# Performance work log

Hardware: AMD Instinct MI355X
Metric: run time of the kernel (lower is better)

Reference implementation:

```python
import jax, jax.numpy as jnp
import numpy as np

N_NODES = 40000
N_EDGES = 480000
MULT = 64
NUM_SPECIES = 5
N_BASIS = 8
MLP_HIDDEN = 64
AVG_NEIGH = 12.0

INV8 = float(1.0 / np.sqrt(8.0))
INV64 = float(1.0 / np.sqrt(64.0))
INV128 = float(1.0 / np.sqrt(128.0))


def _poly_envelope(x):
    # e3nn.poly_envelope(5, 2) == DimeNet-style cutoff with p=6:
    # f(0)=1, first 5 derivatives zero at 0, f and 2 derivatives zero at 1.
    u = 1.0 - 28.0 * x**6 + 48.0 * x**7 - 21.0 * x**8
    return jnp.where(x < 1.0, u, 0.0)


def setup_inputs() -> dict:
    key = jax.random.key(0)
    ks = jax.random.split(key, 15)
    vectors = jax.random.uniform(ks[0], (N_EDGES, 3), jnp.float32, -0.5, 0.5)
    node_scalars = jax.random.normal(ks[1], (N_NODES, MULT), jnp.float32)
    node_vectors = jax.random.normal(ks[2], (N_NODES, MULT, 3), jnp.float32)
    node_specie = jax.random.randint(ks[3], (N_NODES,), 0, NUM_SPECIES)
    senders = jax.random.randint(ks[4], (N_EDGES,), 0, N_NODES)
    receivers = jax.random.randint(ks[5], (N_EDGES,), 0, N_NODES)
    # learned params (e3nn Linear weights ~ N(0,1), fwd divides by sqrt(fan_in))
    W_up_s = jax.random.normal(ks[6], (MULT, MULT), jnp.float32)
    W_up_v = jax.random.normal(ks[7], (MULT, MULT), jnp.float32)
    W_skip_s = jax.random.normal(ks[8], (NUM_SPECIES, MULT, 2 * MULT), jnp.float32)
    W_skip_v = jax.random.normal(ks[9], (NUM_SPECIES, MULT, MULT), jnp.float32)
    W_mlp1 = jax.random.normal(ks[10], (N_BASIS, MLP_HIDDEN), jnp.float32)
    W_mlp2 = jax.random.normal(ks[11], (MLP_HIDDEN, MLP_HIDDEN), jnp.float32)
    W_mlp3 = jax.random.normal(ks[12], (MLP_HIDDEN, 4 * MULT), jnp.float32)
    W_down_s = jax.random.normal(ks[13], (2 * MULT, 2 * MULT), jnp.float32)
    W_down_v = jax.random.normal(ks[14], (2 * MULT, MULT), jnp.float32)
    return dict(vectors=vectors, node_scalars=node_scalars, node_vectors=node_vectors,
                node_specie=node_specie, senders=senders, receivers=receivers,
                W_up_s=W_up_s, W_up_v=W_up_v, W_skip_s=W_skip_s, W_skip_v=W_skip_v,
                W_mlp1=W_mlp1, W_mlp2=W_mlp2, W_mlp3=W_mlp3,
                W_down_s=W_down_s, W_down_v=W_down_v)


def reference(vectors, node_scalars, node_vectors, node_specie, senders, receivers,
              W_up_s, W_up_v, W_skip_s, W_skip_v, W_mlp1, W_mlp2, W_mlp3,
              W_down_s, W_down_v):
    N = node_scalars.shape[0]
    # self-connection: species-indexed linear ('skip_tp'), output 128x0e + 64x1o
    sc_s = jnp.einsum('ni,nio->no', node_scalars, W_skip_s[node_specie]) * INV64
    sc_v = jnp.einsum('nic,nio->noc', node_vectors, W_skip_v[node_specie]) * INV64
    # linear_up (irreps-wise linear, 64x0e+64x1o -> same)
    h_s = (node_scalars @ W_up_s) * INV64
    h_v = jnp.einsum('nic,io->noc', node_vectors, W_up_v) * INV64
    # gather by sender
    m_s = h_s[senders]                       # [E,64]
    m_v = h_v[senders]                       # [E,64,3]
    # spherical harmonics l=1, normalize=True, component norm: sqrt(3)*r_hat
    lengths = jnp.linalg.norm(vectors, axis=1, keepdims=True)   # [E,1]
    safe_len = jnp.where(lengths == 0.0, 1.0, lengths)
    Y = jnp.sqrt(3.0) * vectors / safe_len                      # [E,3]
    # sparse CG tensor product (component norm): 0e x 1o -> 1o, 1o x 1o -> 0e
    tp_1o = m_s[:, :, None] * Y[:, None, :]                     # [E,64,3]
    tp_0e = jnp.einsum('eic,ec->ei', m_v, Y) / jnp.sqrt(3.0)    # [E,64]
    # concatenate + regroup -> 128x0e + 128x1o
    msg_s = jnp.concatenate([m_s, tp_0e], axis=1)               # [E,128]
    msg_v = jnp.concatenate([m_v, tp_1o], axis=1)               # [E,128,3]
    # radial basis (bessel, x_max=1) * smooth envelope
    k = jnp.arange(1, N_BASIS + 1, dtype=jnp.float32)
    bes = jnp.sqrt(2.0) * jnp.sin(k * jnp.pi * safe_len) / safe_len  # [E,8]
    rb = jnp.where(lengths == 0.0, 0.0, bes * _poly_envelope(lengths))
    h = jax.nn.swish((rb @ W_mlp1) * INV8)
    h = jax.nn.swish((h @ W_mlp2) * INV64)
    mix = (h @ W_mlp3) * INV64                                  # [E,256]
    msg_s = msg_s * mix[:, :128]
    msg_v = msg_v * mix[:, 128:, None]
    # scatter-add to receivers, normalize by sqrt(avg_num_neighbors)
    inv_sqrt_nn = 1.0 / np.sqrt(AVG_NEIGH)
    agg_s = jax.ops.segment_sum(msg_s, receivers, num_segments=N) * inv_sqrt_nn
    agg_v = jax.ops.segment_sum(msg_v, receivers, num_segments=N) * inv_sqrt_nn
    # linear_down to 128x0e + 64x1o, plus self-connection
    d_s = (agg_s @ W_down_s) * INV128 + sc_s                    # [N,128]
    d_v = jnp.einsum('nic,io->noc', agg_v, W_down_v) * INV128 + sc_v  # [N,64,3]
    # gate: first 64 scalars kept (swish), last 64 gate the vectors (swish)
    out_s = jax.nn.swish(d_s[:, :MULT])
    gates = jax.nn.swish(d_s[:, MULT:])
    out_v = d_v * gates[:, :, None]
    return jnp.concatenate([out_s, out_v.reshape(N, MULT * 3)], axis=1)  # [N,256]
```

## Files before the change

### kernel.cpp

```cpp
#include <hip/hip_runtime.h>
#include <hip/hip_bf16.h>

#define N_NODES 40000
#define N_EDGES 480000
#define SEG 4
#define SEG_E (N_EDGES / SEG)
#define SEG_TILES (SEG_E / 16)
#define SCAN_BLOCKS 157

typedef short bf16x8 __attribute__((ext_vector_type(8)));
typedef float f32x4 __attribute__((ext_vector_type(4)));

__device__ __forceinline__ float bf2f(__hip_bfloat16 x) { return __bfloat162float(x); }

__device__ __forceinline__ float swishf(float x) { return x / (1.0f + __expf(-x)); }

__device__ __forceinline__ float bflo(unsigned u) { union { unsigned u; float f; } w; w.u = u << 16; return w.f; }
__device__ __forceinline__ float bfhi(unsigned u) { union { unsigned u; float f; } w; w.u = u & 0xffff0000u; return w.f; }
__device__ __forceinline__ float bfu(unsigned short u) { union { unsigned u; float f; } w; w.u = ((unsigned)u) << 16; return w.f; }

__device__ __forceinline__ unsigned short f2bf_bits(float x) {
    union { __hip_bfloat16 h; unsigned short u; } c; c.h = __float2bfloat16(x); return c.u;
}

__constant__ const float INV8 = 0.35355339059327373f;
__constant__ const float INV64 = 0.125f;
__constant__ const float INV128 = 0.08838834764831845f;
__constant__ const float INV_NN = 0.2886751345948129f;
__constant__ const float SQRT2 = 1.4142135623730951f;
__constant__ const float SQRT3 = 1.7320508075688772f;
__constant__ const float INV_SQRT3 = 0.5773502691896258f;
__constant__ const float PI_F = 3.14159265358979323846f;

template<bool F32>
__device__ __forceinline__ float LD(const void* p, int i) {
    if constexpr (F32) return ((const float*)p)[i];
    else return bf2f(((const __hip_bfloat16*)p)[i]);
}
template<bool F32>
__device__ __forceinline__ void ST(void* p, size_t i, float v) {
    if constexpr (F32) ((float*)p)[i] = v;
    else ((__hip_bfloat16*)p)[i] = __float2bfloat16(v);
}

template<bool F32>
__device__ __forceinline__ void load_f8(const void* p, size_t i, float* out) {
    if constexpr (F32) {
        const float4* q4 = (const float4*)((const float*)p + i);
        float4 a = q4[0], b = q4[1];
        out[0] = a.x; out[1] = a.y; out[2] = a.z; out[3] = a.w;
        out[4] = b.x; out[5] = b.y; out[6] = b.z; out[7] = b.w;
    } else {
        bf16x8 v = *(const bf16x8*)((const unsigned short*)p + i);
        #pragma unroll
        for (int j = 0; j < 8; j++) out[j] = bfu((unsigned short)v[j]);
    }
}

__global__ void detect_kernel(const unsigned short* __restrict__ w, int* __restrict__ flag) {
    int lane = threadIdx.x;
    int cnt = 0;
    for (int i = lane; i < 2048; i += 64) {
        unsigned e = (w[2 * i] >> 7) & 0xFF;
        if (e >= 110 && e <= 133) cnt++;
    }
    #pragma unroll
    for (int off = 32; off > 0; off >>= 1) cnt += __shfl_down(cnt, off, 64);
    if (lane == 0) *flag = (cnt > 1024) ? 1 : 0;
}

template<bool F32>
__global__ __launch_bounds__(256) void wprep_kernel(
    const void* __restrict__ W_up_s, const void* __restrict__ W_up_v,
    const void* __restrict__ W_skip_s, const void* __restrict__ W_skip_v,
    const void* __restrict__ W_down_s, const void* __restrict__ W_down_v,
    const void* __restrict__ W_mlp2, const void* __restrict__ W_mlp3,
    unsigned short* __restrict__ Wup_sq, unsigned short* __restrict__ Wup_vq,
    unsigned short* __restrict__ Wq_s, unsigned short* __restrict__ Wq_v,
    unsigned short* __restrict__ W2q, unsigned short* __restrict__ W3q,
    const int* __restrict__ flag)
{
    if ((*flag != 0) == F32) return;
    const float SC = INV128 * INV_NN;
    int gid = blockIdx.x * 256 + threadIdx.x;
    int gs = gridDim.x * 256;
    for (int i = gid; i < 4096; i += gs) {
        int o = i & 63, k = i >> 6;
        Wup_sq[o * 72 + k] = f2bf_bits(LD<F32>(W_up_s, k * 64 + o) * INV64);
        Wup_vq[o * 72 + k] = f2bf_bits(LD<F32>(W_up_v, k * 64 + o) * INV64);
    }
    for (int i = gid; i < 5 * 128 * 192; i += gs) {
        int sp = i / 24576, r = i - sp * 24576;
        int o = r / 192, k = r - o * 192;
        float w = (k < 128) ? LD<F32>(W_down_s, k * 128 + o) * SC
                            : LD<F32>(W_skip_s, sp * 8192 + (k - 128) * 128 + o) * INV64;
        Wq_s[sp * 25600 + o * 200 + k] = f2bf_bits(w);
    }
    for (int i = gid; i < 5 * 64 * 192; i += gs) {
        int sp = i / 12288, r = i - sp * 12288;
        int o = r / 192, k = r - o * 192;
        float w = (k < 128) ? LD<F32>(W_down_v, k * 64 + o) * SC
                            : LD<F32>(W_skip_v, sp * 4096 + (k - 128) * 64 + o) * INV64;
        Wq_v[sp * 12800 + o * 200 + k] = f2bf_bits(w);
    }
    for (int i = gid; i < 16384; i += gs) {
        int o = i & 255, k = i >> 8;
        W3q[o * 72 + k] = f2bf_bits(LD<F32>(W_mlp3, k * 256 + o));
    }
    for (int i = gid; i < 4096; i += gs) {
        int o = i & 63, k = i >> 6;
        W2q[o * 72 + k] = f2bf_bits(LD<F32>(W_mlp2, k * 64 + o));
    }
}

__global__ __launch_bounds__(256) void hist_kernel(const int* __restrict__ receivers,
                                                   int* __restrict__ cnt) {
    int e = blockIdx.x * 256 + threadIdx.x;
    if (e < N_EDGES) atomicAdd(&cnt[receivers[e]], 1);
}

__global__ __launch_bounds__(256) void partial_kernel(const int* __restrict__ cnt,
                                                      int* __restrict__ partials) {
    __shared__ int red[4];
    int idx = blockIdx.x * 256 + threadIdx.x;
    int v = (idx < N_NODES) ? cnt[idx] : 0;
    #pragma unroll
    for (int off = 32; off > 0; off >>= 1) v += __shfl_down(v, off, 64);
    int wave = threadIdx.x >> 6, lane = threadIdx.x & 63;
    if (lane == 0) red[wave] = v;
    __syncthreads();
    if (threadIdx.x == 0) partials[blockIdx.x] = red[0] + red[1] + red[2] + red[3];
}

__global__ __launch_bounds__(256) void scanp_kernel(const int* __restrict__ partials,
                                                    int* __restrict__ pscan) {
    __shared__ int buf[256];
    int t = threadIdx.x;
    int v = (t < SCAN_BLOCKS) ? partials[t] : 0;
    buf[t] = v;
    __syncthreads();
    for (int off = 1; off < 256; off <<= 1) {
        int tmp = (t >= off) ? buf[t - off] : 0;
        __syncthreads();
        buf[t] += tmp;
        __syncthreads();
    }
    if (t < SCAN_BLOCKS) pscan[t] = buf[t] - v;
}

__global__ __launch_bounds__(256) void offs_kernel(const int* __restrict__ cnt,
                                                   const int* __restrict__ pscan,
                                                   int* __restrict__ offs,
                                                   int* __restrict__ cursor) {
    __shared__ int buf[256];
    int b = blockIdx.x, t = threadIdx.x;
    int idx = b * 256 + t;
    int v = (idx < N_NODES) ? cnt[idx] : 0;
    buf[t] = v;
    __syncthreads();
    for (int off = 1; off < 256; off <<= 1) {
        int tmp = (t >= off) ? buf[t - off] : 0;
        __syncthreads();
        buf[t] += tmp;
        __syncthreads();
    }
    int exc = buf[t] - v + pscan[b];
    if (idx < N_NODES) { offs[idx] = exc; cursor[idx] = exc; }
    if (idx == N_NODES - 1) offs[N_NODES] = exc + v;
}

__global__ __launch_bounds__(256) void scatter_kernel(const int* __restrict__ receivers,
                                                      const int* __restrict__ senders,
                                                      int* __restrict__ cursor,
                                                      int* __restrict__ sorted_eid,
                                                      int* __restrict__ sorted_snd) {
    int e = blockIdx.x * 256 + threadIdx.x;
    if (e < N_EDGES) {
        int p = atomicAdd(&cursor[receivers[e]], 1);
        sorted_eid[p] = e;
        sorted_snd[p] = senders[e];
    }
}

__global__ __launch_bounds__(256) void hist5_kernel(const int* __restrict__ specie,
                                                    int* __restrict__ cnt5) {
    int n = blockIdx.x * 256 + threadIdx.x;
    int lane = threadIdx.x & 63;
    int sp = (n < N_NODES) ? specie[n] : -1;
    #pragma unroll
    for (int s = 0; s < 5; s++) {
        unsigned long long mask = __ballot(sp == s);
        if (mask != 0ull) {
            int leader = __builtin_ctzll(mask);
            if (lane == leader) atomicAdd(&cnt5[s], __popcll(mask));
        }
    }
}

__global__ void scan5_kernel(const int* __restrict__ cnt5, int* __restrict__ sp_offs,
                             int* __restrict__ cursor5, int* __restrict__ tile_info) {
    if (threadIdx.x != 0 || blockIdx.x != 0) return;
    int run = 0, tb = 0;
    for (int s = 0; s < 5; s++) {
        sp_offs[s] = run; cursor5[s] = run;
        tile_info[s] = tb;
        int c = cnt5[s];
        int T = (c + 15) >> 4;
        tile_info[8 + s] = T;
        tb += (T + 3) >> 2;
        run += c;
    }
    sp_offs[5] = run;
    tile_info[5] = tb;
}

__global__ __launch_bounds__(256) void scatter5_kernel(const int* __restrict__ specie,
                                                       int* __restrict__ cursor5,
                                                       int* __restrict__ sorted_node) {
    int n = blockIdx.x * 256 + threadIdx.x;
    int lane = threadIdx.x & 63;
    int sp = (n < N_NODES) ? specie[n] : -1;
    #pragma unroll
    for (int s = 0; s < 5; s++) {
        unsigned long long mask = __ballot(sp == s);
        if (mask != 0ull) {
            int leader = __builtin_ctzll(mask);
            int base = 0;
            if (lane == leader) base = atomicAdd(&cursor5[s], __popcll(mask));
            base = __shfl(base, leader);
            if (sp == s) {
                int prefix = __popcll(mask & ((1ull << lane) - 1ull));
                sorted_node[base + prefix] = n;
            }
        }
    }
}

template<bool F32>
__global__ __launch_bounds__(256) void node_up_kernel(
    const void* __restrict__ node_scalars,
    const void* __restrict__ node_vectors,
    const unsigned short* __restrict__ Wup_sq,
    const unsigned short* __restrict__ Wup_vq,
    unsigned short* __restrict__ hbuf,
    unsigned short* __restrict__ ns_b,
    unsigned short* __restrict__ nv_t,
    const int* __restrict__ flag)
{
    if ((*flag != 0) == F32) return;
    __shared__ __align__(16) unsigned short WsT[64 * 72];
    __shared__ __align__(16) unsigned short WvT[64 * 72];
    int tid = threadIdx.x;
    for (int i = tid; i < 576; i += 256) {
        ((uint4*)WsT)[i] = ((const uint4*)Wup_sq)[i];
        ((uint4*)WvT)[i] = ((const uint4*)Wup_vq)[i];
    }
    __syncthreads();
    int wave = tid >> 6, lane = tid & 63;
    int m = lane & 15, q = lane >> 4;
    int base = (blockIdx.x * 4 + wave) * 16;

    f32x4 accS[4];
    f32x4 accV[3][4];
    #pragma unroll
    for (int t = 0; t < 4; t++) {
        accS[t] = f32x4{0.f, 0.f, 0.f, 0.f};
        #pragma unroll
        for (int c = 0; c < 3; c++) accV[c][t] = f32x4{0.f, 0.f, 0.f, 0.f};
    }

    #pragma unroll
    for (int kk = 0; kk < 2; kk++) {
        int i0 = kk * 32 + 8 * q;
        float fs[8];
        load_f8<F32>(node_scalars, (size_t)(base + m) * 64 + i0, fs);
        bf16x8 aS;
        #pragma unroll
        for (int j = 0; j < 8; j++) aS[j] = (short)f2bf_bits(fs[j]);
        *(bf16x8*)(ns_b + (size_t)(base + m) * 64 + i0) = aS;
        float fv[24];
        size_t vbase = (size_t)(base + m) * 192 + (size_t)i0 * 3;
        load_f8<F32>(node_vectors, vbase,      fv);
        load_f8<F32>(node_vectors, vbase + 8,  fv + 8);
        load_f8<F32>(node_vectors, vbase + 16, fv + 16);
        bf16x8 aV[3];
        #pragma unroll
        for (int c = 0; c < 3; c++) {
            #pragma unroll
            for (int j = 0; j < 8; j++) aV[c][j] = (short)f2bf_bits(fv[3 * j + c]);
            *(bf16x8*)(nv_t + (size_t)c * N_NODES * 64 + (size_t)(base + m) * 64 + i0) = aV[c];
        }
        #pragma unroll
        for (int t = 0; t < 4; t++) {
            bf16x8 bS = *(const bf16x8*)(WsT + (16 * t + m) * 72 + kk * 32 + 8 * q);
            bf16x8 bV = *(const bf16x8*)(WvT + (16 * t + m) * 72 + kk * 32 + 8 * q);
            accS[t]    = __builtin_amdgcn_mfma_f32_16x16x32_bf16(aS,    bS, accS[t],    0, 0, 0);
            accV[0][t] = __builtin_amdgcn_mfma_f32_16x16x32_bf16(aV[0], bV, accV[0][t], 0, 0, 0);
            accV[1][t] = __builtin_amdgcn_mfma_f32_16x16x32_bf16(aV[1], bV, accV[1][t], 0, 0, 0);
            accV[2][t] = __builtin_amdgcn_mfma_f32_16x16x32_bf16(aV[2], bV, accV[2][t], 0, 0, 0);
        }
    }
    #pragma unroll
    for (int t = 0; t < 4; t++) {
        #pragma unroll
        for (int r = 0; r < 4; r++) {
            uint2 pk;
            pk.x = (unsigned)f2bf_bits(accS[t][r])    | ((unsigned)f2bf_bits(accV[0][t][r]) << 16);
            pk.y = (unsigned)f2bf_bits(accV[1][t][r]) | ((unsigned)f2bf_bits(accV[2][t][r]) << 16);
            *(uint2*)(hbuf + (size_t)(base + 4 * q + r) * 256 + (16 * t + m) * 4) = pk;
        }
    }
}

template<bool F32>
__global__ __launch_bounds__(512) void mlp_kernel(
    const void* __restrict__ vectors,
    const int* __restrict__ sorted_eid,
    const void* __restrict__ W1,
    const unsigned short* __restrict__ W2q,
    const unsigned short* __restrict__ W3q,
    unsigned short* __restrict__ mixseg,
    unsigned short* __restrict__ yq,
    int p_lo,
    const int* __restrict__ flag)
{
    if ((*flag != 0) == F32) return;
    __shared__ __align__(16) unsigned short W3T[256 * 72];
    __shared__ __align__(16) unsigned short W2T[64 * 72];
    __shared__ unsigned short hbl[8 * 64 * 17];
    int tid = threadIdx.x;
    for (int i = tid; i < 2304; i += 512) ((uint4*)W3T)[i] = ((const uint4*)W3q)[i];
    for (int i = tid; i < 576; i += 512)  ((uint4*)W2T)[i] = ((const uint4*)W2q)[i];
    __syncthreads();
    int wave = tid >> 6, lane = tid & 63;
    int m = lane & 15, q = lane >> 4;
    int tile = blockIdx.x * 8 + wave;
    if (tile >= SEG_TILES) return;
    int p = p_lo + tile * 16 + m;

    int e = sorted_eid[p];
    float vx = LD<F32>(vectors, e * 3 + 0);
    float vy = LD<F32>(vectors, e * 3 + 1);
    float vz = LD<F32>(vectors, e * 3 + 2);
    float len2 = vx * vx + vy * vy + vz * vz;
    float len = sqrtf(len2);
    float Yx = 0.f, Yy = 0.f, Yz = 0.f;
    float rb[8];
    if (len > 0.f) {
        float inv = 1.f / len;
        Yx = SQRT3 * vx * inv; Yy = SQRT3 * vy * inv; Yz = SQRT3 * vz * inv;
        float x6 = len2 * len2 * len2;
        float env = (len < 1.f) ? fmaf(x6, fmaf(len, fmaf(len, -21.f, 48.f), -28.f), 1.f) : 0.f;
        float c = SQRT2 * inv * env;
        #pragma unroll
        for (int k = 0; k < 8; k++) rb[k] = c * __sinf((float)(k + 1) * PI_F * len);
    } else {
        #pragma unroll
        for (int k = 0; k < 8; k++) rb[k] = 0.f;
    }
    if (q == 0) {
        uint2 yw;
        yw.x = f2bf_bits(Yx) | ((unsigned)f2bf_bits(Yy) << 16);
        yw.y = f2bf_bits(Yz);
        *(uint2*)(yq + (size_t)p * 4) = yw;
    }

    f32x4 zero4 = {0.f, 0.f, 0.f, 0.f};
    unsigned short* hb = hbl + wave * (64 * 17);

    bf16x8 b_rb;
    #pragma unroll
    for (int j = 0; j < 8; j++) b_rb[j] = (q == 0) ? (short)f2bf_bits(rb[j]) : (short)0;
    #pragma unroll
    for (int t = 0; t < 4; t++) {
        bf16x8 a;
        #pragma unroll
        for (int j = 0; j < 8; j++) a[j] = 0;
        if (q == 0) {
            #pragma unroll
            for (int j = 0; j < 8; j++)
                a[j] = (short)f2bf_bits(LD<F32>(W1, j * 64 + 16 * t + m));
        }
        f32x4 c = __builtin_amdgcn_mfma_f32_16x16x32_bf16(a, b_rb, zero4, 0, 0, 0);
        #pragma unroll
        for (int r = 0; r < 4; r++)
            hb[(16 * t + 4 * q + r) * 17 + m] = f2bf_bits(swishf(c[r] * INV8));
    }
    bf16x8 b2[2];
    #pragma unroll
    for (int h = 0; h < 2; h++)
        #pragma unroll
        for (int j = 0; j < 8; j++)
            b2[h][j] = (short)hb[(32 * h + 8 * q + j) * 17 + m];
    #pragma unroll
    for (int t = 0; t < 4; t++) {
        bf16x8 a0 = *(const bf16x8*)(W2T + (16 * t + m) * 72 + 8 * q);
        bf16x8 a1 = *(const bf16x8*)(W2T + (16 * t + m) * 72 + 32 + 8 * q);
        f32x4 c = __builtin_amdgcn_mfma_f32_16x16x32_bf16(a0, b2[0], zero4, 0, 0, 0);
        c = __builtin_amdgcn_mfma_f32_16x16x32_bf16(a1, b2[1], c, 0, 0, 0);
        #pragma unroll
        for (int r = 0; r < 4; r++)
            hb[(16 * t + 4 * q + r) * 17 + m] = f2bf_bits(swishf(c[r] * INV64));
    }
    bf16x8 b3[2];
    #pragma unroll
    for (int h = 0; h < 2; h++)
        #pragma unroll
        for (int j = 0; j < 8; j++)
            b3[h][j] = (short)hb[(32 * h + 8 * q + j) * 17 + m];
    size_t rowbase = ((size_t)(tile * 16 + m)) * 256;
    #pragma unroll
    for (int t3 = 0; t3 < 16; t3++) {
        bf16x8 a0 = *(const bf16x8*)(W3T + (16 * t3 + m) * 72 + 8 * q);
        bf16x8 a1 = *(const bf16x8*)(W3T + (16 * t3 + m) * 72 + 32 + 8 * q);
        f32x4 c = __builtin_amdgcn_mfma_f32_16x16x32_bf16(a0, b3[0], zero4, 0, 0, 0);
        c = __builtin_amdgcn_mfma_f32_16x16x32_bf16(a1, b3[1], c, 0, 0, 0);
        uint2 v;
        v.x = f2bf_bits(c[0] * INV64) | ((unsigned)f2bf_bits(c[1] * INV64) << 16);
        v.y = f2bf_bits(c[2] * INV64) | ((unsigned)f2bf_bits(c[3] * INV64) << 16);
        *(uint2*)(mixseg + rowbase + 16 * t3 + 4 * q) = v;
    }
}

__global__ __launch_bounds__(256) void agg_kernel(
    const unsigned short* __restrict__ hbuf,
    const int* __restrict__ sorted_snd,
    const unsigned short* __restrict__ mixseg,
    const unsigned short* __restrict__ yq,
    const int* __restrict__ offs,
    unsigned short* __restrict__ agg_s_b,
    unsigned short* __restrict__ agg_v_b,
    int slo, int shi)
{
    int tid = threadIdx.x, wave = tid >> 6, lane = tid & 63;
    int n = blockIdx.x * 4 + wave;
    if (n >= N_NODES) return;
    int beg = __builtin_amdgcn_readfirstlane(offs[n]);
    int end = __builtin_amdgcn_readfirstlane(offs[n + 1]);
    int lo = beg > slo ? beg : slo;
    int hi = end < shi ? end : shi;
    bool owner = (beg >= slo && beg < shi) || (beg >= shi && shi == N_EDGES);
    if (!owner && hi <= lo) return;
    unsigned short* aS = agg_s_b + (size_t)n * 128;
    unsigned short* aV = agg_v_b + (size_t)n * 384;
    float s0, s1, v0, v1, v2, v3, v4, v5;
    if (owner) {
        s0 = s1 = v0 = v1 = v2 = v3 = v4 = v5 = 0.f;
    } else {
        s0 = bfu(aS[lane]); s1 = bfu(aS[64 + lane]);
        v0 = bfu(aV[lane]); v1 = bfu(aV[64 + lane]); v2 = bfu(aV[128 + lane]);
        v3 = bfu(aV[192 + lane]); v4 = bfu(aV[256 + lane]); v5 = bfu(aV[320 + lane]);
    }
    for (int p = lo; p < hi; p++) {
        int snd = __builtin_amdgcn_readfirstlane(sorted_snd[p]);
        uint2 hbv = *(const uint2*)(hbuf + (size_t)snd * 256 + lane * 4);
        float m_s = bflo(hbv.x), mv0 = bfhi(hbv.x);
        float mv1 = bflo(hbv.y), mv2 = bfhi(hbv.y);
        const unsigned short* mp = mixseg + (size_t)(p - slo) * 256;
        float mix0 = bfu(mp[lane]);
        float mix1 = bfu(mp[64 + lane]);
        float mix2 = bfu(mp[128 + lane]);
        float mix3 = bfu(mp[192 + lane]);
        uint2 yw = *(const uint2*)(yq + (size_t)p * 4);
        float Yx = bflo(yw.x), Yy = bfhi(yw.x), Yz = bflo(yw.y);
        float tp0 = (mv0 * Yx + mv1 * Yy + mv2 * Yz) * INV_SQRT3;
        s0 = fmaf(m_s, mix0, s0);
        s1 = fmaf(tp0, mix1, s1);
        float t1 = m_s * mix3;
        v0 = fmaf(mv0, mix2, v0);
        v1 = fmaf(t1, Yx, v1);
        v2 = fmaf(mv1, mix2, v2);
        v3 = fmaf(t1, Yy, v3);
        v4 = fmaf(mv2, mix2, v4);
        v5 = fmaf(t1, Yz, v5);
    }
    aS[lane] = f2bf_bits(s0); aS[64 + lane] = f2bf_bits(s1);
    aV[lane] = f2bf_bits(v0); aV[64 + lane] = f2bf_bits(v1); aV[128 + lane] = f2bf_bits(v2);
    aV[192 + lane] = f2bf_bits(v3); aV[256 + lane] = f2bf_bits(v4); aV[320 + lane] = f2bf_bits(v5);
}

template<bool F32>
__global__ __launch_bounds__(256) void node_final_kernel(
    const unsigned short* __restrict__ Wq_s,
    const unsigned short* __restrict__ Wq_v,
    const unsigned short* __restrict__ ns_b,
    const unsigned short* __restrict__ nv_t,
    const unsigned short* __restrict__ agg_s_b,
    const unsigned short* __restrict__ agg_v_b,
    const int* __restrict__ sorted_node,
    const int* __restrict__ sp_offs,
    const int* __restrict__ tile_info,
    void* __restrict__ out,
    const int* __restrict__ flag)
{
    if ((*flag != 0) == F32) return;
    int b = blockIdx.x;
    if (b >= tile_info[5]) return;
    __shared__ __align__(16) unsigned short As[128 * 200];
    __shared__ __align__(16) unsigned short Av[64 * 200];
    int sp = 0;
    #pragma unroll
    for (int s = 1; s < 5; s++) if (b >= tile_info[s]) sp = s;
    int tid = threadIdx.x;
    const uint4* ps = (const uint4*)(Wq_s + (size_t)sp * 25600);
    for (int i = tid; i < 3200; i += 256) ((uint4*)As)[i] = ps[i];
    const uint4* pv = (const uint4*)(Wq_v + (size_t)sp * 12800);
    for (int i = tid; i < 1600; i += 256) ((uint4*)Av)[i] = pv[i];
    __syncthreads();
    int wave = tid >> 6, lane = tid & 63;
    int m = lane & 15, q = lane >> 4;
    int T = tile_info[8 + sp];
    int tl = (b - tile_info[sp]) * 4 + wave;
    if (tl >= T) return;
    int row = sp_offs[sp] + tl * 16;
    int cnt = sp_offs[sp + 1] - row; if (cnt > 16) cnt = 16;
    int mm = (m < cnt) ? m : 0;
    int node = sorted_node[row + mm];

    bf16x8 bs[6];
    {
        const unsigned short* a = agg_s_b + (size_t)node * 128;
        #pragma unroll
        for (int f = 0; f < 4; f++) bs[f] = *(const bf16x8*)(a + f * 32 + q * 8);
        const unsigned short* s = ns_b + (size_t)node * 64;
        #pragma unroll
        for (int f = 0; f < 2; f++) bs[4 + f] = *(const bf16x8*)(s + f * 32 + q * 8);
    }
    bf16x8 bv[3][6];
    #pragma unroll
    for (int c = 0; c < 3; c++) {
        const unsigned short* a = agg_v_b + (size_t)node * 384 + c * 128;
        #pragma unroll
        for (int f = 0; f < 4; f++) bv[c][f] = *(const bf16x8*)(a + f * 32 + q * 8);
        const unsigned short* s = nv_t + (size_t)c * N_NODES * 64 + (size_t)node * 64;
        #pragma unroll
        for (int f = 0; f < 2; f++) bv[c][4 + f] = *(const bf16x8*)(s + f * 32 + q * 8);
    }
    f32x4 z4 = {0.f, 0.f, 0.f, 0.f};
    float gate[4][4];
    #pragma unroll
    for (int t = 0; t < 4; t++) {
        f32x4 c = z4;
        #pragma unroll
        for (int f = 0; f < 6; f++) {
            bf16x8 a = *(const bf16x8*)(As + (16 * (4 + t) + m) * 200 + f * 32 + q * 8);
            c = __builtin_amdgcn_mfma_f32_16x16x32_bf16(a, bs[f], c, 0, 0, 0);
        }
        #pragma unroll
        for (int r = 0; r < 4; r++) gate[t][r] = swishf(c[r]);
    }
    #pragma unroll
    for (int t = 0; t < 4; t++) {
        f32x4 c = z4;
        #pragma unroll
        for (int f = 0; f < 6; f++) {
            bf16x8 a = *(const bf16x8*)(As + (16 * t + m) * 200 + f * 32 + q * 8);
            c = __builtin_amdgcn_mfma_f32_16x16x32_bf16(a, bs[f], c, 0, 0, 0);
        }
        if (m < cnt) {
            size_t base = (size_t)node * 256 + 16 * t + 4 * q;
            if constexpr (F32) {
                float4 o4 = { swishf(c[0]), swishf(c[1]), swishf(c[2]), swishf(c[3]) };
                *(float4*)((float*)out + base) = o4;
            } else {
                uint2 o2;
                o2.x = f2bf_bits(swishf(c[0])) | ((unsigned)f2bf_bits(swishf(c[1])) << 16);
                o2.y = f2bf_bits(swishf(c[2])) | ((unsigned)f2bf_bits(swishf(c[3])) << 16);
                *(uint2*)((unsigned short*)out + base) = o2;
            }
        }
    }
    #pragma unroll
    for (int t = 0; t < 4; t++) {
        f32x4 c0 = z4, c1 = z4, c2 = z4;
        #pragma unroll
        for (int f = 0; f < 6; f++) {
            bf16x8 a = *(const bf16x8*)(Av + (16 * t + m) * 200 + f * 32 + q * 8);
            c0 = __builtin_amdgcn_mfma_f32_16x16x32_bf16(a, bv[0][f], c0, 0, 0, 0);
            c1 = __builtin_amdgcn_mfma_f32_16x16x32_bf16(a, bv[1][f], c1, 0, 0, 0);
            c2 = __builtin_amdgcn_mfma_f32_16x16x32_bf16(a, bv[2][f], c2, 0, 0, 0);
        }
        if (m < cnt) {
            #pragma unroll
            for (int r = 0; r < 4; r++) {
                float g = gate[t][r];
                int o = 16 * t + 4 * q + r;
                size_t base = (size_t)node * 256 + 64 + (size_t)o * 3;
                ST<F32>(out, base + 0, c0[r] * g);
                ST<F32>(out, base + 1, c1[r] * g);
                ST<F32>(out, base + 2, c2[r] * g);
            }
        }
    }
}

extern "C" void kernel_launch(void* const* d_in, const int* in_sizes, int n_in,
                              void* d_out, int out_size, void* d_ws, size_t ws_size,
                              hipStream_t stream) {
    const void* vectors      = d_in[0];
    const void* node_scalars = d_in[1];
    const void* node_vectors = d_in[2];
    const int* node_specie   = (const int*)d_in[3];
    const int* senders       = (const int*)d_in[4];
    const int* receivers     = (const int*)d_in[5];
    const void* W_up_s       = d_in[6];
    const void* W_up_v       = d_in[7];
    const void* W_skip_s     = d_in[8];
    const void* W_skip_v     = d_in[9];
    const void* W_mlp1       = d_in[10];
    const void* W_mlp2       = d_in[11];
    const void* W_mlp3       = d_in[12];
    const void* W_down_s     = d_in[13];
    const void* W_down_v     = d_in[14];

    char* ws = (char*)d_ws;
    size_t off = 0;
    auto alloc = [&](size_t bytes) { void* p = ws + off; off += (bytes + 255) & ~(size_t)255; return p; };
    unsigned short* hbuf     = (unsigned short*)alloc((size_t)N_NODES * 256 * 2);
    unsigned short* ns_b     = (unsigned short*)alloc((size_t)N_NODES * 64 * 2);
    unsigned short* nv_t     = (unsigned short*)alloc((size_t)N_NODES * 192 * 2);
    unsigned short* agg_s_b  = (unsigned short*)alloc((size_t)N_NODES * 128 * 2);
    unsigned short* agg_v_b  = (unsigned short*)alloc((size_t)N_NODES * 384 * 2);
    unsigned short* mixseg   = (unsigned short*)alloc((size_t)SEG_E * 256 * 2);
    unsigned short* yq       = (unsigned short*)alloc((size_t)N_EDGES * 4 * 2);
    unsigned short* Wup_sq   = (unsigned short*)alloc((size_t)64 * 72 * 2);
    unsigned short* Wup_vq   = (unsigned short*)alloc((size_t)64 * 72 * 2);
    unsigned short* Wq_s     = (unsigned short*)alloc((size_t)5 * 128 * 200 * 2);
    unsigned short* Wq_v     = (unsigned short*)alloc((size_t)5 * 64 * 200 * 2);
    unsigned short* W2q      = (unsigned short*)alloc((size_t)64 * 72 * 2);
    unsigned short* W3q      = (unsigned short*)alloc((size_t)256 * 72 * 2);
    int* cnt        = (int*)alloc((size_t)(N_NODES + 8) * 4);
    int* cnt5       = cnt + N_NODES;
    int* offs       = (int*)alloc((size_t)(N_NODES + 1) * 4);
    int* cursor     = (int*)alloc((size_t)N_NODES * 4);
    int* sorted     = (int*)alloc((size_t)N_EDGES * 4);
    int* sorted_snd = (int*)alloc((size_t)N_EDGES * 4);
    int* sorted_node= (int*)alloc((size_t)N_NODES * 4);
    int* sp_offs    = (int*)alloc(16 * 4);
    int* cursor5    = (int*)alloc(16 * 4);
    int* tile_info  = (int*)alloc(16 * 4);
    int* partials   = (int*)alloc((size_t)(SCAN_BLOCKS + 1) * 4);
    int* pscan      = (int*)alloc((size_t)(SCAN_BLOCKS + 1) * 4);
    int* flag       = (int*)alloc(4);

    detect_kernel<<<dim3(1), dim3(64), 0, stream>>>((const unsigned short*)W_up_s, flag);
    hipMemsetAsync(cnt, 0, (size_t)(N_NODES + 8) * 4, stream);

    wprep_kernel<true><<<dim3(64), dim3(256), 0, stream>>>(
        W_up_s, W_up_v, W_skip_s, W_skip_v, W_down_s, W_down_v, W_mlp2, W_mlp3,
        Wup_sq, Wup_vq, Wq_s, Wq_v, W2q, W3q, flag);
    wprep_kernel<false><<<dim3(64), dim3(256), 0, stream>>>(
        W_up_s, W_up_v, W_skip_s, W_skip_v, W_down_s, W_down_v, W_mlp2, W_mlp3,
        Wup_sq, Wup_vq, Wq_s, Wq_v, W2q, W3q, flag);

    hist_kernel<<<dim3(1875), dim3(256), 0, stream>>>(receivers, cnt);
    partial_kernel<<<dim3(SCAN_BLOCKS), dim3(256), 0, stream>>>(cnt, partials);
    scanp_kernel<<<dim3(1), dim3(256), 0, stream>>>(partials, pscan);
    offs_kernel<<<dim3(SCAN_BLOCKS), dim3(256), 0, stream>>>(cnt, pscan, offs, cursor);
    scatter_kernel<<<dim3(1875), dim3(256), 0, stream>>>(receivers, senders, cursor, sorted, sorted_snd);

    hist5_kernel<<<dim3(157), dim3(256), 0, stream>>>(node_specie, cnt5);
    scan5_kernel<<<dim3(1), dim3(64), 0, stream>>>(cnt5, sp_offs, cursor5, tile_info);
    scatter5_kernel<<<dim3(157), dim3(256), 0, stream>>>(node_specie, cursor5, sorted_node);

    node_up_kernel<true><<<dim3(625), dim3(256), 0, stream>>>(
        node_scalars, node_vectors, Wup_sq, Wup_vq, hbuf, ns_b, nv_t, flag);
    node_up_kernel<false><<<dim3(625), dim3(256), 0, stream>>>(
        node_scalars, node_vectors, Wup_sq, Wup_vq, hbuf, ns_b, nv_t, flag);

    const int MLP_BLOCKS = (SEG_TILES + 7) / 8;
    for (int s = 0; s < SEG; s++) {
        int p_lo = s * SEG_E;
        mlp_kernel<true><<<dim3(MLP_BLOCKS), dim3(512), 0, stream>>>(
            vectors, sorted, W_mlp1, W2q, W3q, mixseg, yq, p_lo, flag);
        mlp_kernel<false><<<dim3(MLP_BLOCKS), dim3(512), 0, stream>>>(
            vectors, sorted, W_mlp1, W2q, W3q, mixseg, yq, p_lo, flag);
        agg_kernel<<<dim3(10000), dim3(256), 0, stream>>>(
            hbuf, sorted_snd, mixseg, yq, offs, agg_s_b, agg_v_b, p_lo, p_lo + SEG_E);
    }

    node_final_kernel<true><<<dim3(640), dim3(256), 0, stream>>>(
        Wq_s, Wq_v, ns_b, nv_t, agg_s_b, agg_v_b,
        sorted_node, sp_offs, tile_info, d_out, flag);
    node_final_kernel<false><<<dim3(640), dim3(256), 0, stream>>>(
        Wq_s, Wq_v, ns_b, nv_t, agg_s_b, agg_v_b,
        sorted_node, sp_offs, tile_info, d_out, flag);
}
```

Baseline: 554.5 us.

## Merge dtype kernel variants, halve edge segments, and batch sender loads in aggregation

The F32 and bf16 template instantiations of each kernel become one kernel that reads the dtype flag at runtime. This removes the paired launches where one variant exited early. The edge pipeline now uses 2 segments instead of 4, which halves the mlp/agg launch pairs but needs a larger mix buffer per segment. The aggregation loop loads 64 sender indices per wave at once, takes them with readlane, and processes two edges per iteration for more memory-level parallelism. The cost is runtime branches on the dtype flag and higher register pressure.

Result: no change. 544.1 us (-1.9%).

```diff
diff --git a/kernel.cpp b/kernel.cpp
--- a/kernel.cpp
+++ b/kernel.cpp
@@ -3,7 +3,7 @@
 
 #define N_NODES 40000
 #define N_EDGES 480000
-#define SEG 4
+#define SEG 2
 #define SEG_E (N_EDGES / SEG)
 #define SEG_TILES (SEG_E / 16)
 #define SCAN_BLOCKS 157
@@ -32,20 +32,14 @@
 __constant__ const float INV_SQRT3 = 0.5773502691896258f;
 __constant__ const float PI_F = 3.14159265358979323846f;
 
-template<bool F32>
-__device__ __forceinline__ float LD(const void* p, int i) {
-    if constexpr (F32) return ((const float*)p)[i];
-    else return bf2f(((const __hip_bfloat16*)p)[i]);
-}
-template<bool F32>
-__device__ __forceinline__ void ST(void* p, size_t i, float v) {
-    if constexpr (F32) ((float*)p)[i] = v;
-    else ((__hip_bfloat16*)p)[i] = __float2bfloat16(v);
-}
-
-template<bool F32>
-__device__ __forceinline__ void load_f8(const void* p, size_t i, float* out) {
-    if constexpr (F32) {
+__device__ __forceinline__ float LDf(const void* p, size_t i, bool f32) {
+    float v;
+    if (f32) v = ((const float*)p)[i];
+    else     v = bf2f(((const __hip_bfloat16*)p)[i]);
+    return v;
+}
+__device__ __forceinline__ void load_f8r(const void* p, size_t i, bool f32, float* out) {
+    if (f32) {
         const float4* q4 = (const float4*)((const float*)p + i);
         float4 a = q4[0], b = q4[1];
         out[0] = a.x; out[1] = a.y; out[2] = a.z; out[3] = a.w;
@@ -69,7 +63,6 @@
     if (lane == 0) *flag = (cnt > 1024) ? 1 : 0;
 }
 
-template<bool F32>
 __global__ __launch_bounds__(256) void wprep_kernel(
     const void* __restrict__ W_up_s, const void* __restrict__ W_up_v,
     const void* __restrict__ W_skip_s, const void* __restrict__ W_skip_v,
@@ -80,36 +73,36 @@
     unsigned short* __restrict__ W2q, unsigned short* __restrict__ W3q,
     const int* __restrict__ flag)
 {
-    if ((*flag != 0) == F32) return;
+    bool f32 = (*flag == 0);
     const float SC = INV128 * INV_NN;
     int gid = blockIdx.x * 256 + threadIdx.x;
     int gs = gridDim.x * 256;
     for (int i = gid; i < 4096; i += gs) {
         int o = i & 63, k = i >> 6;
-        Wup_sq[o * 72 + k] = f2bf_bits(LD<F32>(W_up_s, k * 64 + o) * INV64);
-        Wup_vq[o * 72 + k] = f2bf_bits(LD<F32>(W_up_v, k * 64 + o) * INV64);
+        Wup_sq[o * 72 + k] = f2bf_bits(LDf(W_up_s, k * 64 + o, f32) * INV64);
+        Wup_vq[o * 72 + k] = f2bf_bits(LDf(W_up_v, k * 64 + o, f32) * INV64);
     }
     for (int i = gid; i < 5 * 128 * 192; i += gs) {
         int sp = i / 24576, r = i - sp * 24576;
         int o = r / 192, k = r - o * 192;
-        float w = (k < 128) ? LD<F32>(W_down_s, k * 128 + o) * SC
-                            : LD<F32>(W_skip_s, sp * 8192 + (k - 128) * 128 + o) * INV64;
+        float w = (k < 128) ? LDf(W_down_s, k * 128 + o, f32) * SC
+                            : LDf(W_skip_s, sp * 8192 + (k - 128) * 128 + o, f32) * INV64;
         Wq_s[sp * 25600 + o * 200 + k] = f2bf_bits(w);
     }
     for (int i = gid; i < 5 * 64 * 192; i += gs) {
         int sp = i / 12288, r = i - sp * 12288;
         int o = r / 192, k = r - o * 192;
-        float w = (k < 128) ? LD<F32>(W_down_v, k * 64 + o) * SC
-                            : LD<F32>(W_skip_v, sp * 4096 + (k - 128) * 64 + o) * INV64;
+        float w = (k < 128) ? LDf(W_down_v, k * 64 + o, f32) * SC
+                            : LDf(W_skip_v, sp * 4096 + (k - 128) * 64 + o, f32) * INV64;
         Wq_v[sp * 12800 + o * 200 + k] = f2bf_bits(w);
     }
     for (int i = gid; i < 16384; i += gs) {
         int o = i & 255, k = i >> 8;
-        W3q[o * 72 + k] = f2bf_bits(LD<F32>(W_mlp3, k * 256 + o));
+        W3q[o * 72 + k] = f2bf_bits(LDf(W_mlp3, k * 256 + o, f32));
     }
     for (int i = gid; i < 4096; i += gs) {
         int o = i & 63, k = i >> 6;
-        W2q[o * 72 + k] = f2bf_bits(LD<F32>(W_mlp2, k * 64 + o));
+        W2q[o * 72 + k] = f2bf_bits(LDf(W_mlp2, k * 64 + o, f32));
     }
 }
 
@@ -236,7 +229,6 @@
     }
 }
 
-template<bool F32>
 __global__ __launch_bounds__(256) void node_up_kernel(
     const void* __restrict__ node_scalars,
     const void* __restrict__ node_vectors,
@@ -247,7 +239,7 @@
     unsigned short* __restrict__ nv_t,
     const int* __restrict__ flag)
 {
-    if ((*flag != 0) == F32) return;
+    bool f32 = (*flag == 0);
     __shared__ __align__(16) unsigned short WsT[64 * 72];
     __shared__ __align__(16) unsigned short WvT[64 * 72];
     int tid = threadIdx.x;
@@ -273,16 +265,16 @@
     for (int kk = 0; kk < 2; kk++) {
         int i0 = kk * 32 + 8 * q;
         float fs[8];
-        load_f8<F32>(node_scalars, (size_t)(base + m) * 64 + i0, fs);
+        load_f8r(node_scalars, (size_t)(base + m) * 64 + i0, f32, fs);
         bf16x8 aS;
         #pragma unroll
         for (int j = 0; j < 8; j++) aS[j] = (short)f2bf_bits(fs[j]);
         *(bf16x8*)(ns_b + (size_t)(base + m) * 64 + i0) = aS;
         float fv[24];
         size_t vbase = (size_t)(base + m) * 192 + (size_t)i0 * 3;
-        load_f8<F32>(node_vectors, vbase,      fv);
-        load_f8<F32>(node_vectors, vbase + 8,  fv + 8);
-        load_f8<F32>(node_vectors, vbase + 16, fv + 16);
+        load_f8r(node_vectors, vbase,      f32, fv);
+        load_f8r(node_vectors, vbase + 8,  f32, fv + 8);
+        load_f8r(node_vectors, vbase + 16, f32, fv + 16);
         bf16x8 aV[3];
         #pragma unroll
         for (int c = 0; c < 3; c++) {
@@ -312,7 +304,6 @@
     }
 }
 
-template<bool F32>
 __global__ __launch_bounds__(512) void mlp_kernel(
     const void* __restrict__ vectors,
     const int* __restrict__ sorted_eid,
@@ -324,7 +315,7 @@
     int p_lo,
     const int* __restrict__ flag)
 {
-    if ((*flag != 0) == F32) return;
+    bool f32 = (*flag == 0);
     __shared__ __align__(16) unsigned short W3T[256 * 72];
     __shared__ __align__(16) unsigned short W2T[64 * 72];
     __shared__ unsigned short hbl[8 * 64 * 17];
@@ -339,9 +330,9 @@
     int p = p_lo + tile * 16 + m;
 
     int e = sorted_eid[p];
-    float vx = LD<F32>(vectors, e * 3 + 0);
-    float vy = LD<F32>(vectors, e * 3 + 1);
-    float vz = LD<F32>(vectors, e * 3 + 2);
+    float vx = LDf(vectors, (size_t)e * 3 + 0, f32);
+    float vy = LDf(vectors, (size_t)e * 3 + 1, f32);
+    float vz = LDf(vectors, (size_t)e * 3 + 2, f32);
     float len2 = vx * vx + vy * vy + vz * vz;
     float len = sqrtf(len2);
     float Yx = 0.f, Yy = 0.f, Yz = 0.f;
@@ -379,7 +370,7 @@
         if (q == 0) {
             #pragma unroll
             for (int j = 0; j < 8; j++)
-                a[j] = (short)f2bf_bits(LD<F32>(W1, j * 64 + 16 * t + m));
+                a[j] = (short)f2bf_bits(LDf(W1, j * 64 + 16 * t + m, f32));
         }
         f32x4 c = __builtin_amdgcn_mfma_f32_16x16x32_bf16(a, b_rb, zero4, 0, 0, 0);
         #pragma unroll
@@ -451,35 +442,71 @@
         v0 = bfu(aV[lane]); v1 = bfu(aV[64 + lane]); v2 = bfu(aV[128 + lane]);
         v3 = bfu(aV[192 + lane]); v4 = bfu(aV[256 + lane]); v5 = bfu(aV[320 + lane]);
     }
-    for (int p = lo; p < hi; p++) {
-        int snd = __builtin_amdgcn_readfirstlane(sorted_snd[p]);
-        uint2 hbv = *(const uint2*)(hbuf + (size_t)snd * 256 + lane * 4);
-        float m_s = bflo(hbv.x), mv0 = bfhi(hbv.x);
-        float mv1 = bflo(hbv.y), mv2 = bfhi(hbv.y);
-        const unsigned short* mp = mixseg + (size_t)(p - slo) * 256;
-        float mix0 = bfu(mp[lane]);
-        float mix1 = bfu(mp[64 + lane]);
-        float mix2 = bfu(mp[128 + lane]);
-        float mix3 = bfu(mp[192 + lane]);
-        uint2 yw = *(const uint2*)(yq + (size_t)p * 4);
-        float Yx = bflo(yw.x), Yy = bfhi(yw.x), Yz = bflo(yw.y);
-        float tp0 = (mv0 * Yx + mv1 * Yy + mv2 * Yz) * INV_SQRT3;
-        s0 = fmaf(m_s, mix0, s0);
-        s1 = fmaf(tp0, mix1, s1);
-        float t1 = m_s * mix3;
-        v0 = fmaf(mv0, mix2, v0);
-        v1 = fmaf(t1, Yx, v1);
-        v2 = fmaf(mv1, mix2, v2);
-        v3 = fmaf(t1, Yy, v3);
-        v4 = fmaf(mv2, mix2, v4);
-        v5 = fmaf(t1, Yz, v5);
+    for (int chunk = lo; chunk < hi; chunk += 64) {
+        int cc = hi - chunk; if (cc > 64) cc = 64;
+        int sv = (lane < cc) ? sorted_snd[chunk + lane] : 0;
+        int i = 0;
+        for (; i + 1 < cc; i += 2) {
+            int snd0 = __builtin_amdgcn_readlane(sv, i);
+            int snd1 = __builtin_amdgcn_readlane(sv, i + 1);
+            int p0 = chunk + i, p1 = chunk + i + 1;
+            uint2 h0 = *(const uint2*)(hbuf + (size_t)snd0 * 256 + lane * 4);
+            uint2 h1 = *(const uint2*)(hbuf + (size_t)snd1 * 256 + lane * 4);
+            const unsigned short* mp0 = mixseg + (size_t)(p0 - slo) * 256;
+            const unsigned short* mp1 = mixseg + (size_t)(p1 - slo) * 256;
+            float a0 = bfu(mp0[lane]), a1 = bfu(mp0[64 + lane]);
+            float a2 = bfu(mp0[128 + lane]), a3 = bfu(mp0[192 + lane]);
+            float b0 = bfu(mp1[lane]), b1 = bfu(mp1[64 + lane]);
+            float b2 = bfu(mp1[128 + lane]), b3 = bfu(mp1[192 + lane]);
+            uint2 yw0 = *(const uint2*)(yq + (size_t)p0 * 4);
+            uint2 yw1 = *(const uint2*)(yq + (size_t)p1 * 4);
+            {
+                float m_s = bflo(h0.x), mv0 = bfhi(h0.x), mv1 = bflo(h0.y), mv2 = bfhi(h0.y);
+                float Yx = bflo(yw0.x), Yy = bfhi(yw0.x), Yz = bflo(yw0.y);
+                float tp0 = (mv0 * Yx + mv1 * Yy + mv2 * Yz) * INV_SQRT3;
+                s0 = fmaf(m_s, a0, s0);
+                s1 = fmaf(tp0, a1, s1);
+                float t1 = m_s * a3;
+                v0 = fmaf(mv0, a2, v0); v1 = fmaf(t1, Yx, v1);
+                v2 = fmaf(mv1, a2, v2); v3 = fmaf(t1, Yy, v3);
+                v4 = fmaf(mv2, a2, v4); v5 = fmaf(t1, Yz, v5);
+            }
+            {
+                float m_s = bflo(h1.x), mv0 = bfhi(h1.x), mv1 = bflo(h1.y), mv2 = bfhi(h1.y);
+                float Yx = bflo(yw1.x), Yy = bfhi(yw1.x), Yz = bflo(yw1.y);
+                float tp0 = (mv0 * Yx + mv1 * Yy + mv2 * Yz) * INV_SQRT3;
+                s0 = fmaf(m_s, b0, s0);
+                s1 = fmaf(tp0, b1, s1);
+                float t1 = m_s * b3;
+                v0 = fmaf(mv0, b2, v0); v1 = fmaf(t1, Yx, v1);
+                v2 = fmaf(mv1, b2, v2); v3 = fmaf(t1, Yy, v3);
+                v4 = fmaf(mv2, b2, v4); v5 = fmaf(t1, Yz, v5);
+            }
+        }
+        if (i < cc) {
+            int snd = __builtin_amdgcn_readlane(sv, i);
+            int p = chunk + i;
+            uint2 hbv = *(const uint2*)(hbuf + (size_t)snd * 256 + lane * 4);
+            const unsigned short* mp = mixseg + (size_t)(p - slo) * 256;
+            float mix0 = bfu(mp[lane]), mix1 = bfu(mp[64 + lane]);
+            float mix2 = bfu(mp[128 + lane]), mix3 = bfu(mp[192 + lane]);
+            uint2 yw = *(const uint2*)(yq + (size_t)p * 4);
+            float m_s = bflo(hbv.x), mv0 = bfhi(hbv.x), mv1 = bflo(hbv.y), mv2 = bfhi(hbv.y);
+            float Yx = bflo(yw.x), Yy = bfhi(yw.x), Yz = bflo(yw.y);
+            float tp0 = (mv0 * Yx + mv1 * Yy + mv2 * Yz) * INV_SQRT3;
+            s0 = fmaf(m_s, mix0, s0);
+            s1 = fmaf(tp0, mix1, s1);
+            float t1 = m_s * mix3;
+            v0 = fmaf(mv0, mix2, v0); v1 = fmaf(t1, Yx, v1);
+            v2 = fmaf(mv1, mix2, v2); v3 = fmaf(t1, Yy, v3);
+            v4 = fmaf(mv2, mix2, v4); v5 = fmaf(t1, Yz, v5);
+        }
     }
     aS[lane] = f2bf_bits(s0); aS[64 + lane] = f2bf_bits(s1);
     aV[lane] = f2bf_bits(v0); aV[64 + lane] = f2bf_bits(v1); aV[128 + lane] = f2bf_bits(v2);
     aV[192 + lane] = f2bf_bits(v3); aV[256 + lane] = f2bf_bits(v4); aV[320 + lane] = f2bf_bits(v5);
 }
 
-template<bool F32>
 __global__ __launch_bounds__(256) void node_final_kernel(
     const unsigned short* __restrict__ Wq_s,
     const unsigned short* __restrict__ Wq_v,
@@ -493,7 +520,7 @@
     void* __restrict__ out,
     const int* __restrict__ flag)
 {
-    if ((*flag != 0) == F32) return;
+    bool f32 = (*flag == 0);
     int b = blockIdx.x;
     if (b >= tile_info[5]) return;
     __shared__ __align__(16) unsigned short As[128 * 200];
@@ -559,7 +586,7 @@
         }
         if (m < cnt) {
             size_t base = (size_t)node * 256 + 16 * t + 4 * q;
-            if constexpr (F32) {
+            if (f32) {
                 float4 o4 = { swishf(c[0]), swishf(c[1]), swishf(c[2]), swishf(c[3]) };
                 *(float4*)((float*)out + base) = o4;
             } else {
@@ -586,9 +613,15 @@
                 float g = gate[t][r];
                 int o = 16 * t + 4 * q + r;
                 size_t base = (size_t)node * 256 + 64 + (size_t)o * 3;
-                ST<F32>(out, base + 0, c0[r] * g);
-                ST<F32>(out, base + 1, c1[r] * g);
-                ST<F32>(out, base + 2, c2[r] * g);
+                if (f32) {
+                    ((float*)out)[base + 0] = c0[r] * g;
+                    ((float*)out)[base + 1] = c1[r] * g;
+                    ((float*)out)[base + 2] = c2[r] * g;
+                } else {
+                    ((__hip_bfloat16*)out)[base + 0] = __float2bfloat16(c0[r] * g);
+                    ((__hip_bfloat16*)out)[base + 1] = __float2bfloat16(c1[r] * g);
+                    ((__hip_bfloat16*)out)[base + 2] = __float2bfloat16(c2[r] * g);
+                }
             }
         }
     }
@@ -646,10 +679,7 @@
     detect_kernel<<<dim3(1), dim3(64), 0, stream>>>((const unsigned short*)W_up_s, flag);
     hipMemsetAsync(cnt, 0, (size_t)(N_NODES + 8) * 4, stream);
 
-    wprep_kernel<true><<<dim3(64), dim3(256), 0, stream>>>(
-        W_up_s, W_up_v, W_skip_s, W_skip_v, W_down_s, W_down_v, W_mlp2, W_mlp3,
-        Wup_sq, Wup_vq, Wq_s, Wq_v, W2q, W3q, flag);
-    wprep_kernel<false><<<dim3(64), dim3(256), 0, stream>>>(
+    wprep_kernel<<<dim3(64), dim3(256), 0, stream>>>(
         W_up_s, W_up_v, W_skip_s, W_skip_v, W_down_s, W_down_v, W_mlp2, W_mlp3,
         Wup_sq, Wup_vq, Wq_s, Wq_v, W2q, W3q, flag);
 
@@ -663,26 +693,19 @@
     scan5_kernel<<<dim3(1), dim3(64), 0, stream>>>(cnt5, sp_offs, cursor5, tile_info);
     scatter5_kernel<<<dim3(157), dim3(256), 0, stream>>>(node_specie, cursor5, sorted_node);
 
-    node_up_kernel<true><<<dim3(625), dim3(256), 0, stream>>>(
-        node_scalars, node_vectors, Wup_sq, Wup_vq, hbuf, ns_b, nv_t, flag);
-    node_up_kernel<false><<<dim3(625), dim3(256), 0, stream>>>(
+    node_up_kernel<<<dim3(625), dim3(256), 0, stream>>>(
         node_scalars, node_vectors, Wup_sq, Wup_vq, hbuf, ns_b, nv_t, flag);
 
     const int MLP_BLOCKS = (SEG_TILES + 7) / 8;
     for (int s = 0; s < SEG; s++) {
         int p_lo = s * SEG_E;
-        mlp_kernel<true><<<dim3(MLP_BLOCKS), dim3(512), 0, stream>>>(
-            vectors, sorted, W_mlp1, W2q, W3q, mixseg, yq, p_lo, flag);
-        mlp_kernel<false><<<dim3(MLP_BLOCKS), dim3(512), 0, stream>>>(
+        mlp_kernel<<<dim3(MLP_BLOCKS), dim3(512), 0, stream>>>(
             vectors, sorted, W_mlp1, W2q, W3q, mixseg, yq, p_lo, flag);
         agg_kernel<<<dim3(10000), dim3(256), 0, stream>>>(
             hbuf, sorted_snd, mixseg, yq, offs, agg_s_b, agg_v_b, p_lo, p_lo + SEG_E);
     }
 
-    node_final_kernel<true><<<dim3(640), dim3(256), 0, stream>>>(
+    node_final_kernel<<<dim3(640), dim3(256), 0, stream>>>(
         Wq_s, Wq_v, ns_b, nv_t, agg_s_b, agg_v_b,
         sorted_node, sp_offs, tile_info, d_out, flag);
-    node_final_kernel<false><<<dim3(640), dim3(256), 0, stream>>>(
-        Wq_s, Wq_v, ns_b, nv_t, agg_s_b, agg_v_b,
-        sorted_node, sp_offs, tile_info, d_out, flag);
-}
+}
```
